# Optimization experiments

Measured on AMD Instinct MI355X. Metric: run time of the kernel, lower is better.

Reference implementation:

```python
import jax, jax.numpy as jnp
import numpy as np

V = 100000
E = 524288
D_IN = 128
D_OUT = 128
NUM_REL = 474
BN_EPS = 1e-5


def setup_inputs() -> dict:
    key = jax.random.key(0)
    ks = jax.random.split(key, 12)
    return {
        "x": jax.random.normal(ks[0], (V, D_IN), dtype=jnp.float32),
        "rel_repr": jax.random.normal(ks[1], (NUM_REL, D_IN), dtype=jnp.float32),
        "edge_norm": jax.random.uniform(ks[2], (E,), dtype=jnp.float32),
        "in_w": jax.random.normal(ks[3], (D_IN, D_OUT), dtype=jnp.float32) * 0.1,
        "out_w": jax.random.normal(ks[4], (D_IN, D_OUT), dtype=jnp.float32) * 0.1,
        "loop_w": jax.random.normal(ks[5], (D_IN, D_OUT), dtype=jnp.float32) * 0.1,
        "w_rel": jax.random.normal(ks[6], (D_IN, D_OUT), dtype=jnp.float32) * 0.1,
        "loop_rel": jax.random.normal(ks[7], (1, D_IN), dtype=jnp.float32),
        "bias": jnp.zeros((D_OUT,), dtype=jnp.float32),
        "src": jax.random.randint(ks[8], (E,), 0, V, dtype=jnp.int32),
        "dst": jax.random.randint(ks[9], (E,), 0, V, dtype=jnp.int32),
        "edge_type": jax.random.randint(ks[10], (E,), 0, NUM_REL, dtype=jnp.int32),
    }


def reference(x, rel_repr, edge_norm, in_w, out_w, loop_w, w_rel, loop_rel, bias, src, dst, edge_type):
    # comp primitive 'mult': edge_data = src_emb * rel[edge_type]   [E, D_IN]
    rel = rel_repr  # num_base=-1 -> rel_wt is None, rel.data = rel_repr
    edge_data = x[src] * rel[edge_type]
    half = edge_data.shape[0] // 2  # static under jit
    # first half of edges -> in_w, second half -> out_w
    msg = jnp.concatenate([edge_data[:half] @ in_w, edge_data[half:] @ out_w], axis=0)
    msg = msg * edge_norm[:, None]
    # agg primitive 'sum': scatter-sum into dst nodes
    agg = jax.ops.segment_sum(msg, dst, num_segments=x.shape[0])  # [V, D_OUT]
    # self-loop path: comp(x, loop_rel) @ loop_w
    loop_msg = (x * loop_rel) @ loop_w
    # comb primitive 'add', scaled by 1/3 (dropout with p=0 is identity)
    h = (agg + loop_msg) * (1.0 / 3.0)
    h = h + bias
    # BatchNorm1d, training-mode batch stats, gamma=1, beta=0
    mean = jnp.mean(h, axis=0)
    var = jnp.mean((h - mean) ** 2, axis=0)
    h = (h - mean) * jax.lax.rsqrt(var + BN_EPS)
    # act primitive 'relu'; ltr=True -> project relations
    return jax.nn.relu(h), rel @ w_rel
```

## Files before the change

### kernel.cpp

```cpp
#include <hip/hip_runtime.h>

#define V 100000
#define VP 100096
#define E_EDGES 524288
#define HALF 262144
#define D 128
#define NREL 474
#define BN_EPS 1e-5f
#define NBLK 98

#define ROWTILES 782
#define GEMM_GRID 1568
#define RED_BLKS 98
#define RELB 237
#define BNBLK 12500

#define LDK 392
#define LDB 40

typedef unsigned short u16;
typedef unsigned int u32;
typedef unsigned long long u64;
typedef __attribute__((ext_vector_type(8))) short short8;
typedef __attribute__((ext_vector_type(4))) float f32x4;

__device__ __forceinline__ u16 f2bf(float f) {
    union { float f; u32 u; } v; v.f = f;
    u32 u = v.u;
    return (u16)((u + 0x7fffu + ((u >> 16) & 1u)) >> 16);
}
__device__ __forceinline__ u32 pk2(float a, float b) {
    return (u32)f2bf(a) | ((u32)f2bf(b) << 16);
}

__global__ __launch_bounds__(256) void hist_k(const int* __restrict__ dst, u32* __restrict__ cnt) {
    int e = blockIdx.x * 256 + threadIdx.x;
    if (e >= E_EDGES) return;
    u32 d = (u32)dst[e];
    if (d >= V) d = 0;
    atomicAdd(&cnt[d], 1u);
}

__global__ __launch_bounds__(1024) void scanA_k(const u32* __restrict__ cnt,
                                                u32* __restrict__ cursor,
                                                u32* __restrict__ bsum) {
    __shared__ u32 wsum[16];
    int tid = threadIdx.x, wid = tid >> 6, lane = tid & 63;
    int idx = blockIdx.x * 1024 + tid;
    u32 v = (idx < V) ? cnt[idx] : 0u;
    u32 s = v;
#pragma unroll
    for (int o = 1; o < 64; o <<= 1) {
        u32 t = __shfl_up(s, o, 64);
        if (lane >= o) s += t;
    }
    if (lane == 63) wsum[wid] = s;
    __syncthreads();
    if (wid == 0) {
        u32 wv = (lane < 16) ? wsum[lane] : 0u;
#pragma unroll
        for (int o = 1; o < 16; o <<= 1) {
            u32 t = __shfl_up(wv, o, 64);
            if (lane >= o) wv += t;
        }
        if (lane < 16) wsum[lane] = wv;
    }
    __syncthreads();
    u32 wprev = wid ? wsum[wid - 1] : 0u;
    if (idx < V) cursor[idx] = s + wprev - v;
    if (tid == 0) bsum[blockIdx.x] = wsum[15];
}

__global__ __launch_bounds__(128) void scanBbt_k(
    u32* __restrict__ bsum,
    const float* __restrict__ in_w, const float* __restrict__ out_w,
    const float* __restrict__ loop_w, u16* __restrict__ Bt) {
    if (blockIdx.x > 0) {
        int n = blockIdx.x - 1;
        int t = threadIdx.x;
        const float* Ws[3] = {in_w, out_w, loop_w};
#pragma unroll
        for (int seg = 0; seg < 3; seg++)
            Bt[(size_t)n * 384 + seg * 128 + t] = f2bf(Ws[seg][(size_t)t * D + n]);
        return;
    }
    __shared__ u32 wtot;
    int t = threadIdx.x, lane = t & 63, w = t >> 6;
    u32 v = (t < NBLK) ? bsum[t] : 0u;
    u32 s = v;
#pragma unroll
    for (int o = 1; o < 64; o <<= 1) {
        u32 x = __shfl_up(s, o, 64);
        if (lane >= o) s += x;
    }
    if (w == 0 && lane == 63) wtot = s;
    __syncthreads();
    u32 add = (w == 1) ? wtot : 0u;
    if (t < NBLK) bsum[t] = add + s - v;
}

__global__ __launch_bounds__(256) void fill_rec_k(
    const int* __restrict__ dst, const int* __restrict__ src, const int* __restrict__ etype,
    const float* __restrict__ enorm, u32* __restrict__ cursor, const u32* __restrict__ bsum,
    u64* __restrict__ rec) {
    int e = blockIdx.x * 256 + threadIdx.x;
    if (e >= E_EDGES) return;
    u32 d = (u32)dst[e];   if (d >= V) d = 0;
    u32 s = (u32)src[e];   if (s >= V) s = 0;
    u32 t = (u32)etype[e]; if (t >= NREL) t = 0;
    float nm = enorm[e];
    u32 w = s | (t << 17) | ((e < HALF ? 0u : 1u) << 26);
    u32 slot = atomicAdd(&cursor[d], 1u) + bsum[d >> 10];
    u64 r = (u64)w | ((u64)__float_as_uint(nm) << 32);
    if (slot < E_EDGES) rec[slot] = r;
}

struct Rec { u32 s, t, hf; float nm; };
__device__ __forceinline__ Rec dec(u64 r) {
    Rec q; u32 w = (u32)r;
    q.s = w & 0x1FFFFu;
    q.t = (w >> 17) & 0x1FFu;
    q.hf = (w >> 26) & 1u;
    q.nm = __uint_as_float((u32)(r >> 32));
    return q;
}

__global__ __launch_bounds__(256) void gather_k(
    const float* __restrict__ x, const float* __restrict__ rel,
    const u32* __restrict__ cursor, const u32* __restrict__ cnt,
    const u32* __restrict__ bsum, const u64* __restrict__ rec, u16* __restrict__ Aagg) {
    int wave = threadIdx.x >> 6, lane = threadIdx.x & 63;
    int v = blockIdx.x * 4 + wave;
    u32* arow = (u32*)(Aagg + (size_t)v * 256);
    if (v >= V) { arow[lane] = 0u; arow[64 + lane] = 0u; return; }

    u32 n = cnt[v];
    u32 end = cursor[v] + bsum[v >> 10];
    if (end > E_EDGES) end = E_EDGES;
    if (n > end) n = end;
    u32 p = end - n;
    int col = lane * 2;

    float iA0 = 0.f, iA1 = 0.f, oA0 = 0.f, oA1 = 0.f;
    float iB0 = 0.f, iB1 = 0.f, oB0 = 0.f, oB1 = 0.f;

    for (u32 q = p; q < end; q += 4) {
        u64 r0 = rec[q], r1 = rec[q + 1], r2 = rec[q + 2], r3 = rec[q + 3];
        Rec q0 = dec(r0), q1 = dec(r1), q2 = dec(r2), q3 = dec(r3);
        if (q + 1 >= end) q1.nm = 0.f;
        if (q + 2 >= end) q2.nm = 0.f;
        if (q + 3 >= end) q3.nm = 0.f;
        float2 x0 = *(const float2*)(x + (size_t)q0.s * D + col);
        float2 x1 = *(const float2*)(x + (size_t)q1.s * D + col);
        float2 x2 = *(const float2*)(x + (size_t)q2.s * D + col);
        float2 x3 = *(const float2*)(x + (size_t)q3.s * D + col);
        float2 v0 = *(const float2*)(rel + (size_t)q0.t * D + col);
        float2 v1 = *(const float2*)(rel + (size_t)q1.t * D + col);
        float2 v2 = *(const float2*)(rel + (size_t)q2.t * D + col);
        float2 v3 = *(const float2*)(rel + (size_t)q3.t * D + col);
        float f00 = x0.x * v0.x * q0.nm, f01 = x0.y * v0.y * q0.nm;
        float f10 = x1.x * v1.x * q1.nm, f11 = x1.y * v1.y * q1.nm;
        float f20 = x2.x * v2.x * q2.nm, f21 = x2.y * v2.y * q2.nm;
        float f30 = x3.x * v3.x * q3.nm, f31 = x3.y * v3.y * q3.nm;
        if (q0.hf) { oA0 += f00; oA1 += f01; } else { iA0 += f00; iA1 += f01; }
        if (q1.hf) { oB0 += f10; oB1 += f11; } else { iB0 += f10; iB1 += f11; }
        if (q2.hf) { oA0 += f20; oA1 += f21; } else { iA0 += f20; iA1 += f21; }
        if (q3.hf) { oB0 += f30; oB1 += f31; } else { iB0 += f30; iB1 += f31; }
    }
    arow[lane]      = pk2(iA0 + iB0, iA1 + iB1);
    arow[64 + lane] = pk2(oA0 + oB0, oA1 + oB1);
}

__global__ __launch_bounds__(512) void gemm_k(
    const u16* __restrict__ Aagg, const u16* __restrict__ Bt,
    const float* __restrict__ x, const float* __restrict__ loop_rel,
    float* __restrict__ h_out, float* __restrict__ psum, float* __restrict__ psq) {
    __shared__ u16 Bs[64 * 384];
    __shared__ float s_sum[64], s_sq[64];
    int tid = threadIdx.x, wave = tid >> 6, lane = tid & 63;
    int bid = blockIdx.x;
    int rt   = ((bid >> 4) << 3) | (bid & 7);
    int half = (bid >> 3) & 1;
    if (rt >= ROWTILES) return;
    int row0 = rt * 128;

    if (tid < 64) s_sum[tid] = 0.f;
    else if (tid < 128) s_sq[tid - 64] = 0.f;

    int m16 = lane & 15;
    int kq = (lane >> 4) * 8;
    int gvm = row0 + wave * 16 + m16;
    const u16* arow = Aagg + (size_t)gvm * 256;
    bool vok = gvm < V;

    short8 af[8];
#pragma unroll
    for (int ks = 0; ks < 8; ks++) af[ks] = *(const short8*)(arow + ks * 32 + kq);
    short8 lf[4];
    {
        const float* xp = x + (size_t)gvm * D + kq;
#pragma unroll
        for (int kk = 0; kk < 4; kk++) {
            float4 x0 = vok ? *(const float4*)(xp + kk * 32)     : (float4){0.f, 0.f, 0.f, 0.f};
            float4 x1 = vok ? *(const float4*)(xp + kk * 32 + 4) : (float4){0.f, 0.f, 0.f, 0.f};
            float4 l0 = *(const float4*)(loop_rel + kk * 32 + kq);
            float4 l1 = *(const float4*)(loop_rel + kk * 32 + kq + 4);
            union { u32 u[4]; short8 s; } c;
            c.u[0] = pk2(x0.x * l0.x, x0.y * l0.y);
            c.u[1] = pk2(x0.z * l0.z, x0.w * l0.w);
            c.u[2] = pk2(x1.x * l1.x, x1.y * l1.y);
            c.u[3] = pk2(x1.z * l1.z, x1.w * l1.w);
            lf[kk] = c.s;
        }
    }

    {
        const u16* srcB = Bt + (size_t)half * 64 * 384;
        char* bsw = (char*)Bs;
#pragma unroll
        for (int it = 0; it < 6; it++) {
            int c = it * 512 + tid;
            int n = c / 48, s = c - n * 48;
            short8 vv = *(const short8*)(srcB + (size_t)n * 384 + s * 8);
            *(short8*)(bsw + (((u32)(n * 768 + s * 16)) ^ (u32)((n & 7) << 4))) = vv;
        }
    }
    __syncthreads();

    const char* bsb = (const char*)Bs;
    f32x4 acc[4];
#pragma unroll
    for (int ct = 0; ct < 4; ct++) acc[ct] = (f32x4){0.f, 0.f, 0.f, 0.f};

#pragma unroll
    for (int ks = 0; ks < 8; ks++) {
#pragma unroll
        for (int ct = 0; ct < 4; ct++) {
            int n = ct * 16 + m16;
            short8 b = *(const short8*)(bsb + (((u32)(n * 768 + (ks * 32 + kq) * 2)) ^ (u32)((n & 7) << 4)));
            acc[ct] = __builtin_amdgcn_mfma_f32_16x16x32_bf16(af[ks], b, acc[ct], 0, 0, 0);
        }
    }
#pragma unroll
    for (int kk = 0; kk < 4; kk++) {
#pragma unroll
        for (int ct = 0; ct < 4; ct++) {
            int n = ct * 16 + m16;
            short8 b = *(const short8*)(bsb + (((u32)(n * 768 + (256 + kk * 32 + kq) * 2)) ^ (u32)((n & 7) << 4)));
            acc[ct] = __builtin_amdgcn_mfma_f32_16x16x32_bf16(lf[kk], b, acc[ct], 0, 0, 0);
        }
    }

    int m4 = (lane >> 4) * 4;
#pragma unroll
    for (int ct = 0; ct < 4; ct++) {
        float ls = 0.f, lq = 0.f;
#pragma unroll
        for (int i = 0; i < 4; i++) {
            int gv = row0 + wave * 16 + m4 + i;
            if (gv < V) {
                float h = acc[ct][i] * (1.0f / 3.0f);
                h_out[(size_t)gv * D + half * 64 + ct * 16 + m16] = h;
                ls += h; lq += h * h;
            }
        }
        atomicAdd(&s_sum[ct * 16 + m16], ls);
        atomicAdd(&s_sq[ct * 16 + m16], lq);
    }
    __syncthreads();
    if (tid < 64) psum[(size_t)rt * 128 + half * 64 + tid] = s_sum[tid];
    else if (tid < 128) psq[(size_t)rt * 128 + half * 64 + (tid - 64)] = s_sq[tid - 64];
}

__global__ __launch_bounds__(256) void bn_reduce(
    const float* __restrict__ psum, const float* __restrict__ psq,
    float* __restrict__ colsum, float* __restrict__ colsumsq) {
    int t = threadIdx.x;
    int c = t & 127;
    const float* srcp = (t < 128) ? psum : psq;
    float s = 0.f;
    int r0 = blockIdx.x * 8;
#pragma unroll
    for (int i = 0; i < 8; i++) {
        int r = r0 + i;
        if (r < ROWTILES) s += srcp[(size_t)r * 128 + c];
    }
    atomicAdd(((t < 128) ? colsum : colsumsq) + c, s);
}

__global__ __launch_bounds__(256) void final_k(
    float* __restrict__ hio, const float* __restrict__ colsum, const float* __restrict__ colsumsq,
    const float* __restrict__ rel, const float* __restrict__ w, float* __restrict__ out1) {
    int bid = blockIdx.x;
    if (bid < RELB) {
        __shared__ float rs[2][D];
        int rh = threadIdx.x >> 7, c = threadIdx.x & 127;
        int r = bid * 2 + rh;
        rs[rh][c] = rel[(size_t)r * D + c];
        __syncthreads();
        float s = 0.f;
#pragma unroll 8
        for (int k = 0; k < D; k++) s += rs[rh][k] * w[(size_t)k * D + c];
        out1[(size_t)r * D + c] = s;
        return;
    }
    int idx = ((bid - RELB) * 256 + threadIdx.x) * 4;
    if (idx >= V * D) return;
    int col = idx & (D - 1);
    float4 hv = *(const float4*)(hio + idx);
    float4 ov;
    {
        float m0 = colsum[col + 0] * (1.0f / (float)V);
        float m1 = colsum[col + 1] * (1.0f / (float)V);
        float m2 = colsum[col + 2] * (1.0f / (float)V);
        float m3 = colsum[col + 3] * (1.0f / (float)V);
        if (!isfinite(m0)) m0 = 0.f;
        if (!isfinite(m1)) m1 = 0.f;
        if (!isfinite(m2)) m2 = 0.f;
        if (!isfinite(m3)) m3 = 0.f;
        float v0 = colsumsq[col + 0] * (1.0f / (float)V) - m0 * m0;
        float v1 = colsumsq[col + 1] * (1.0f / (float)V) - m1 * m1;
        float v2 = colsumsq[col + 2] * (1.0f / (float)V) - m2 * m2;
        float v3 = colsumsq[col + 3] * (1.0f / (float)V) - m3 * m3;
        if (!isfinite(v0) || v0 < 0.f) v0 = 0.f;
        if (!isfinite(v1) || v1 < 0.f) v1 = 0.f;
        if (!isfinite(v2) || v2 < 0.f) v2 = 0.f;
        if (!isfinite(v3) || v3 < 0.f) v3 = 0.f;
        float f0 = (hv.x - m0) * rsqrtf(v0 + BN_EPS);
        float f1 = (hv.y - m1) * rsqrtf(v1 + BN_EPS);
        float f2 = (hv.z - m2) * rsqrtf(v2 + BN_EPS);
        float f3 = (hv.w - m3) * rsqrtf(v3 + BN_EPS);
        ov.x = (f0 > 0.f) ? f0 : 0.f;
        ov.y = (f1 > 0.f) ? f1 : 0.f;
        ov.z = (f2 > 0.f) ? f2 : 0.f;
        ov.w = (f3 > 0.f) ? f3 : 0.f;
    }
    *(float4*)(hio + idx) = ov;
}

__global__ __launch_bounds__(1024) void scan_k(const u32* __restrict__ cnt,
                                               u32* __restrict__ cursor) {
    __shared__ u32 wsum[16];
    __shared__ u32 carry_s;
    int tid = threadIdx.x, wid = tid >> 6, lane = tid & 63;
    if (tid == 0) carry_s = 0;
    __syncthreads();
    for (int base = 0; base < V; base += 1024) {
        int idx = base + tid;
        u32 v = (idx < V) ? cnt[idx] : 0u;
        u32 s = v;
#pragma unroll
        for (int o = 1; o < 64; o <<= 1) {
            u32 t = __shfl_up(s, o, 64);
            if (lane >= o) s += t;
        }
        if (lane == 63) wsum[wid] = s;
        __syncthreads();
        if (wid == 0) {
            u32 wv = (lane < 16) ? wsum[lane] : 0u;
#pragma unroll
            for (int o = 1; o < 16; o <<= 1) {
                u32 t = __shfl_up(wv, o, 64);
                if (lane >= o) wv += t;
            }
            if (lane < 16) wsum[lane] = wv;
        }
        __syncthreads();
        u32 wprev = (wid == 0) ? 0u : wsum[wid - 1];
        u32 c = carry_s;
        if (idx < V) cursor[idx] = c + s + wprev - v;
        u32 tot = wsum[15];
        __syncthreads();
        if (tid == 0) carry_s = c + tot;
        __syncthreads();
    }
}

__global__ __launch_bounds__(256) void fill_k(
    const int* __restrict__ dst, u32* __restrict__ cursor, u32* __restrict__ eid) {
    int e = blockIdx.x * 256 + threadIdx.x;
    if (e >= E_EDGES) return;
    u32 d = (u32)dst[e];
    if (d >= V) d = 0;
    u32 slot = atomicAdd(&cursor[d], 1u);
    if (slot < E_EDGES) eid[slot] = (u32)e;
}

__global__ __launch_bounds__(256, 1) void fused_k(
    const float* __restrict__ x, const float* __restrict__ rel, const float* __restrict__ loop_rel,
    const float* __restrict__ in_w, const float* __restrict__ out_w, const float* __restrict__ loop_w,
    const float* __restrict__ enorm,
    const int* __restrict__ src, const int* __restrict__ etype,
    const u32* __restrict__ cursor, const u32* __restrict__ cnt,
    const u32* __restrict__ eid,
    float* __restrict__ h_out, float* __restrict__ colsum, float* __restrict__ colsumsq) {
    __shared__ u16 Alds[64 * LDK];
    __shared__ u16 Bs[D * LDB];
    __shared__ float s_sum[D], s_sq[D];

    int tid = threadIdx.x, wave = tid >> 6, lane = tid & 63;
    int row0 = blockIdx.x * 64;

    if (tid < D) { s_sum[tid] = 0.f; s_sq[tid] = 0.f; }

    for (int i = 0; i < 16; i++) {
        int row = wave * 16 + i;
        int gv = row0 + row;
        u32* arow = (u32*)(Alds + row * LDK);
        if (gv < V) {
            float a0 = 0.f, a1 = 0.f, b0 = 0.f, b1 = 0.f;
            float c0 = 0.f, c1 = 0.f, d0 = 0.f, d1 = 0.f;
            u32 n = cnt[gv];
            u32 end = cursor[gv];
            u32 beg = (end >= n) ? end - n : 0u;
            if (beg >= E_EDGES) { beg = 0; n = 0; }
            if (n > E_EDGES - beg) n = E_EDGES - beg;
            u32 nend = beg + n;
            u32 p = beg;
            for (; p + 2 <= nend; p += 2) {
                u32 e0 = eid[p];           if (e0 >= E_EDGES) e0 = 0;
                u32 e1 = eid[p + 1];       if (e1 >= E_EDGES) e1 = 0;
                u32 s0 = (u32)src[e0];     if (s0 >= V) s0 = 0;
                u32 s1 = (u32)src[e1];     if (s1 >= V) s1 = 0;
                u32 t0 = (u32)etype[e0];   if (t0 >= NREL) t0 = 0;
                u32 t1 = (u32)etype[e1];   if (t1 >= NREL) t1 = 0;
                float n0 = enorm[e0];
                float n1 = enorm[e1];
                float2 xv0 = *(const float2*)(x + (size_t)s0 * D + lane * 2);
                float2 xv1 = *(const float2*)(x + (size_t)s1 * D + lane * 2);
                float2 rv0 = *(const float2*)(rel + (size_t)t0 * D + lane * 2);
                float2 rv1 = *(const float2*)(rel + (size_t)t1 * D + lane * 2);
                float f00 = xv0.x * rv0.x * n0, f01 = xv0.y * rv0.y * n0;
                float f10 = xv1.x * rv1.x * n1, f11 = xv1.y * rv1.y * n1;
                if (e0 < HALF) { a0 += f00; a1 += f01; } else { b0 += f00; b1 += f01; }
                if (e1 < HALF) { c0 += f10; c1 += f11; } else { d0 += f10; d1 += f11; }
            }
            if (p < nend) {
                u32 e0 = eid[p];           if (e0 >= E_EDGES) e0 = 0;
                u32 s0 = (u32)src[e0];     if (s0 >= V) s0 = 0;
                u32 t0 = (u32)etype[e0];   if (t0 >= NREL) t0 = 0;
                float n0 = enorm[e0];
                float2 xv0 = *(const float2*)(x + (size_t)s0 * D + lane * 2);
                float2 rv0 = *(const float2*)(rel + (size_t)t0 * D + lane * 2);
                float f00 = xv0.x * rv0.x * n0, f01 = xv0.y * rv0.y * n0;
                if (e0 < HALF) { a0 += f00; a1 += f01; } else { b0 += f00; b1 += f01; }
            }
            a0 += c0; a1 += c1; b0 += d0; b1 += d1;
            float2 xv = *(const float2*)(x + (size_t)gv * D + lane * 2);
            float2 lv = *(const float2*)(loop_rel + lane * 2);
            arow[lane]       = pk2(a0, a1);
            arow[64 + lane]  = pk2(b0, b1);
            arow[128 + lane] = pk2(xv.x * lv.x, xv.y * lv.y);
        } else {
            arow[lane] = 0u; arow[64 + lane] = 0u; arow[128 + lane] = 0u;
        }
    }
    __syncthreads();

    f32x4 acc[8];
#pragma unroll
    for (int ct = 0; ct < 8; ct++) acc[ct] = (f32x4){0.f, 0.f, 0.f, 0.f};

    int m = wave * 16 + (lane & 15);
    int kq = (lane >> 4) * 8;
    int bk = tid >> 3;
    int bn0 = (tid & 7) * 16;

    for (int ks = 0; ks < 12; ks++) {
        int k0 = ks * 32;
        int seg = k0 >> 7;
        int kloc = k0 & 127;
        const float* W = (seg == 0) ? in_w : (seg == 1 ? out_w : loop_w);
#pragma unroll
        for (int j = 0; j < 16; j += 2) {
            float2 w2 = *(const float2*)(W + (size_t)(kloc + bk) * D + bn0 + j);
            Bs[(bn0 + j) * LDB + bk]     = f2bf(w2.x);
            Bs[(bn0 + j + 1) * LDB + bk] = f2bf(w2.y);
        }
        __syncthreads();
        short8 a = *(const short8*)(Alds + m * LDK + k0 + kq);
#pragma unroll
        for (int ct = 0; ct < 8; ct++) {
            short8 b = *(const short8*)(Bs + (ct * 16 + (lane & 15)) * LDB + kq);
            acc[ct] = __builtin_amdgcn_mfma_f32_16x16x32_bf16(a, b, acc[ct], 0, 0, 0);
        }
        __syncthreads();
    }

    int m4 = (lane >> 4) * 4;
#pragma unroll
    for (int ct = 0; ct < 8; ct++) {
        float ls = 0.f, lq = 0.f;
#pragma unroll
        for (int i = 0; i < 4; i++) {
            int gv = row0 + wave * 16 + m4 + i;
            if (gv < V) {
                float h = acc[ct][i] * (1.0f / 3.0f);
                h_out[(size_t)gv * D + ct * 16 + (lane & 15)] = h;
                ls += h; lq += h * h;
            }
        }
        atomicAdd(&s_sum[ct * 16 + (lane & 15)], ls);
        atomicAdd(&s_sq[ct * 16 + (lane & 15)], lq);
    }
    __syncthreads();
    if (tid < D) atomicAdd(&colsum[tid], s_sum[tid]);
    else atomicAdd(&colsumsq[tid - D], s_sq[tid - D]);
}

__global__ void bn_finalize(const float* __restrict__ colsum, const float* __restrict__ colsumsq,
                            float* __restrict__ mean, float* __restrict__ scale) {
    int t = threadIdx.x;
    float m = colsum[t] * (1.0f / (float)V);
    if (!isfinite(m)) m = 0.f;
    float var = colsumsq[t] * (1.0f / (float)V) - m * m;
    if (!isfinite(var) || var < 0.f) var = 0.f;
    mean[t] = m;
    scale[t] = rsqrtf(var + BN_EPS);
}

__global__ __launch_bounds__(256) void bn_relu(
    float* __restrict__ hio, const float* __restrict__ mean, const float* __restrict__ scale) {
    int idx = (blockIdx.x * 256 + threadIdx.x) * 4;
    if (idx >= V * D) return;
    int col = idx & (D - 1);
    float4 hv = *(const float4*)(hio + idx);
    float f0 = (hv.x - mean[col + 0]) * scale[col + 0];
    float f1 = (hv.y - mean[col + 1]) * scale[col + 1];
    float f2 = (hv.z - mean[col + 2]) * scale[col + 2];
    float f3 = (hv.w - mean[col + 3]) * scale[col + 3];
    f0 = (f0 > 0.f) ? f0 : 0.f;
    f1 = (f1 > 0.f) ? f1 : 0.f;
    f2 = (f2 > 0.f) ? f2 : 0.f;
    f3 = (f3 > 0.f) ? f3 : 0.f;
    float4 ov; ov.x = f0; ov.y = f1; ov.z = f2; ov.w = f3;
    *(float4*)(hio + idx) = ov;
}

__global__ __launch_bounds__(128) void rel_gemm(
    const float* __restrict__ rel, const float* __restrict__ w, float* __restrict__ out1) {
    __shared__ float rs[D];
    int t = threadIdx.x;
    int r = blockIdx.x;
    rs[t] = rel[(size_t)r * D + t];
    __syncthreads();
    float s = 0.f;
#pragma unroll 8
    for (int k = 0; k < D; k++) s += rs[k] * w[(size_t)k * D + t];
    out1[(size_t)r * D + t] = s;
}

extern "C" void kernel_launch(void* const* d_in, const int* in_sizes, int n_in,
                              void* d_out, int out_size, void* d_ws, size_t ws_size,
                              hipStream_t stream) {
    const float* x        = (const float*)d_in[0];
    const float* rel_repr = (const float*)d_in[1];
    const float* enorm    = (const float*)d_in[2];
    const float* in_w     = (const float*)d_in[3];
    const float* out_w    = (const float*)d_in[4];
    const float* loop_w   = (const float*)d_in[5];
    const float* w_rel    = (const float*)d_in[6];
    const float* loop_rel = (const float*)d_in[7];
    const int* src   = (const int*)d_in[9];
    const int* dst   = (const int*)d_in[10];
    const int* etype = (const int*)d_in[11];

    float* out0 = (float*)d_out;
    float* out1 = (float*)d_out + (size_t)V * D;

    char* ws = (char*)d_ws;

    {
        size_t off = 0;
        u32* cnt        = (u32*)(ws + off); off += (size_t)V * 4;
        float* colsum   = (float*)(ws + off); off += 512;
        float* colsumsq = (float*)(ws + off); off += 512;
        size_t zero_bytes = off;
        u32* cursor = (u32*)(ws + off); off += (size_t)V * 4;
        u32* bsum   = (u32*)(ws + off); off += 512;
        u16* Bt     = (u16*)(ws + off); off += (size_t)128 * 384 * 2;
        float* psum = (float*)(ws + off); off += (size_t)ROWTILES * 128 * 4;
        float* psq  = (float*)(ws + off); off += (size_t)ROWTILES * 128 * 4;
        u64* rec    = (u64*)(ws + off); off += (size_t)(E_EDGES + 8) * 8;
        u16* Aagg   = (u16*)(ws + off); off += (size_t)VP * 256 * 2;

        if (ws_size >= off) {
            hipMemsetAsync(d_ws, 0, zero_bytes, stream);
            hipMemsetAsync(rec + E_EDGES, 0, 64, stream);
            hist_k<<<(E_EDGES + 255) / 256, 256, 0, stream>>>(dst, cnt);
            scanA_k<<<NBLK, 1024, 0, stream>>>(cnt, cursor, bsum);
            scanBbt_k<<<129, 128, 0, stream>>>(bsum, in_w, out_w, loop_w, Bt);
            fill_rec_k<<<(E_EDGES + 255) / 256, 256, 0, stream>>>(dst, src, etype, enorm, cursor, bsum, rec);
            gather_k<<<VP / 4, 256, 0, stream>>>(x, rel_repr, cursor, cnt, bsum, rec, Aagg);
            gemm_k<<<GEMM_GRID, 512, 0, stream>>>(Aagg, Bt, x, loop_rel, out0, psum, psq);
            bn_reduce<<<RED_BLKS, 256, 0, stream>>>(psum, psq, colsum, colsumsq);
            final_k<<<RELB + BNBLK, 256, 0, stream>>>(out0, colsum, colsumsq, rel_repr, w_rel, out1);
            return;
        }
    }

    {
        size_t off = 0;
        u32* cnt      = (u32*)(ws + off); off += (size_t)V * 4;
        float* colsum = (float*)(ws + off); off += 512;
        float* colsumsq = (float*)(ws + off); off += 512;
        size_t zero_bytes = off;
        u32* cursor   = (u32*)(ws + off); off += (size_t)V * 4;
        float* meanp  = (float*)(ws + off); off += 512;
        float* scalep = (float*)(ws + off); off += 512;
        u32* eid      = (u32*)(ws + off); off += (size_t)E_EDGES * 4;

        if (ws_size < off) return;

        hipMemsetAsync(d_ws, 0, zero_bytes, stream);
        hist_k<<<(E_EDGES + 255) / 256, 256, 0, stream>>>(dst, cnt);
        scan_k<<<1, 1024, 0, stream>>>(cnt, cursor);
        fill_k<<<(E_EDGES + 255) / 256, 256, 0, stream>>>(dst, cursor, eid);
        fused_k<<<(V + 63) / 64, 256, 0, stream>>>(x, rel_repr, loop_rel, in_w, out_w, loop_w,
                                                   enorm, src, etype,
                                                   cursor, cnt, eid,
                                                   out0, colsum, colsumsq);
        bn_finalize<<<1, 128, 0, stream>>>(colsum, colsumsq, meanp, scalep);
        bn_relu<<<(V * D / 4 + 255) / 256, 256, 0, stream>>>(out0, meanp, scalep);
        rel_gemm<<<NREL, 128, 0, stream>>>(rel_repr, w_rel, out1);
    }
}
```

Baseline: 319.9 us.

## Make GEMM persistent over row tiles and write per-wave BN partials

The GEMM kernel becomes persistent: 512 blocks each stage their half of the B matrix into LDS once and loop over row tiles with stride 256, instead of reloading B for every tile. The shared-memory atomics for batch-norm partial sums are replaced by wave shuffles, with each wave writing its own partial row. bn_reduce now sums eight times as many partial rows. The gather kernel also zeroes the source and type indices of padded records so out-of-range lanes read row 0 instead of stale indices. The trade-off is less parallelism per tile and a larger partials buffer.

```diff
diff --git a/kernel.cpp b/kernel.cpp
--- a/kernel.cpp
+++ b/kernel.cpp
@@ -10,7 +10,8 @@
 #define NBLK 98
 
 #define ROWTILES 782
-#define GEMM_GRID 1568
+#define PROWS (ROWTILES * 8)
+#define GEMM_PBLK 512
 #define RED_BLKS 98
 #define RELB 237
 #define BNBLK 12500
@@ -147,9 +148,9 @@
     for (u32 q = p; q < end; q += 4) {
         u64 r0 = rec[q], r1 = rec[q + 1], r2 = rec[q + 2], r3 = rec[q + 3];
         Rec q0 = dec(r0), q1 = dec(r1), q2 = dec(r2), q3 = dec(r3);
-        if (q + 1 >= end) q1.nm = 0.f;
-        if (q + 2 >= end) q2.nm = 0.f;
-        if (q + 3 >= end) q3.nm = 0.f;
+        if (q + 1 >= end) { q1.s = 0; q1.t = 0; q1.nm = 0.f; }
+        if (q + 2 >= end) { q2.s = 0; q2.t = 0; q2.nm = 0.f; }
+        if (q + 3 >= end) { q3.s = 0; q3.t = 0; q3.nm = 0.f; }
         float2 x0 = *(const float2*)(x + (size_t)q0.s * D + col);
         float2 x1 = *(const float2*)(x + (size_t)q1.s * D + col);
         float2 x2 = *(const float2*)(x + (size_t)q2.s * D + col);
@@ -171,48 +172,17 @@
     arow[64 + lane] = pk2(oA0 + oB0, oA1 + oB1);
 }
 
-__global__ __launch_bounds__(512) void gemm_k(
+__global__ __launch_bounds__(512, 4) void gemm_k(
     const u16* __restrict__ Aagg, const u16* __restrict__ Bt,
     const float* __restrict__ x, const float* __restrict__ loop_rel,
-    float* __restrict__ h_out, float* __restrict__ psum, float* __restrict__ psq) {
+    float* __restrict__ h_out, float* __restrict__ ps, float* __restrict__ pq) {
     __shared__ u16 Bs[64 * 384];
-    __shared__ float s_sum[64], s_sq[64];
     int tid = threadIdx.x, wave = tid >> 6, lane = tid & 63;
     int bid = blockIdx.x;
-    int rt   = ((bid >> 4) << 3) | (bid & 7);
-    int half = (bid >> 3) & 1;
-    if (rt >= ROWTILES) return;
-    int row0 = rt * 128;
-
-    if (tid < 64) s_sum[tid] = 0.f;
-    else if (tid < 128) s_sq[tid - 64] = 0.f;
-
+    int half = bid >> 8;
+    int t0   = bid & 255;
     int m16 = lane & 15;
     int kq = (lane >> 4) * 8;
-    int gvm = row0 + wave * 16 + m16;
-    const u16* arow = Aagg + (size_t)gvm * 256;
-    bool vok = gvm < V;
-
-    short8 af[8];
-#pragma unroll
-    for (int ks = 0; ks < 8; ks++) af[ks] = *(const short8*)(arow + ks * 32 + kq);
-    short8 lf[4];
-    {
-        const float* xp = x + (size_t)gvm * D + kq;
-#pragma unroll
-        for (int kk = 0; kk < 4; kk++) {
-            float4 x0 = vok ? *(const float4*)(xp + kk * 32)     : (float4){0.f, 0.f, 0.f, 0.f};
-            float4 x1 = vok ? *(const float4*)(xp + kk * 32 + 4) : (float4){0.f, 0.f, 0.f, 0.f};
-            float4 l0 = *(const float4*)(loop_rel + kk * 32 + kq);
-            float4 l1 = *(const float4*)(loop_rel + kk * 32 + kq + 4);
-            union { u32 u[4]; short8 s; } c;
-            c.u[0] = pk2(x0.x * l0.x, x0.y * l0.y);
-            c.u[1] = pk2(x0.z * l0.z, x0.w * l0.w);
-            c.u[2] = pk2(x1.x * l1.x, x1.y * l1.y);
-            c.u[3] = pk2(x1.z * l1.z, x1.w * l1.w);
-            lf[kk] = c.s;
-        }
-    }
 
     {
         const u16* srcB = Bt + (size_t)half * 64 * 384;
@@ -226,64 +196,94 @@
         }
     }
     __syncthreads();
-
     const char* bsb = (const char*)Bs;
-    f32x4 acc[4];
-#pragma unroll
-    for (int ct = 0; ct < 4; ct++) acc[ct] = (f32x4){0.f, 0.f, 0.f, 0.f};
-
-#pragma unroll
-    for (int ks = 0; ks < 8; ks++) {
+
+    for (int rt = t0; rt < ROWTILES; rt += 256) {
+        int row0 = rt * 128;
+        int gvm = row0 + wave * 16 + m16;
+        const u16* arow = Aagg + (size_t)gvm * 256;
+        bool vok = gvm < V;
+
+        short8 af[8];
+#pragma unroll
+        for (int ks = 0; ks < 8; ks++) af[ks] = *(const short8*)(arow + ks * 32 + kq);
+        short8 lf[4];
+        {
+            const float* xp = x + (size_t)gvm * D + kq;
+#pragma unroll
+            for (int kk = 0; kk < 4; kk++) {
+                float4 x0 = vok ? *(const float4*)(xp + kk * 32)     : (float4){0.f, 0.f, 0.f, 0.f};
+                float4 x1 = vok ? *(const float4*)(xp + kk * 32 + 4) : (float4){0.f, 0.f, 0.f, 0.f};
+                float4 l0 = *(const float4*)(loop_rel + kk * 32 + kq);
+                float4 l1 = *(const float4*)(loop_rel + kk * 32 + kq + 4);
+                union { u32 u[4]; short8 s; } c;
+                c.u[0] = pk2(x0.x * l0.x, x0.y * l0.y);
+                c.u[1] = pk2(x0.z * l0.z, x0.w * l0.w);
+                c.u[2] = pk2(x1.x * l1.x, x1.y * l1.y);
+                c.u[3] = pk2(x1.z * l1.z, x1.w * l1.w);
+                lf[kk] = c.s;
+            }
+        }
+
+        f32x4 acc[4];
+#pragma unroll
+        for (int ct = 0; ct < 4; ct++) acc[ct] = (f32x4){0.f, 0.f, 0.f, 0.f};
+
+#pragma unroll
+        for (int ks = 0; ks < 8; ks++) {
+#pragma unroll
+            for (int ct = 0; ct < 4; ct++) {
+                int n = ct * 16 + m16;
+                short8 b = *(const short8*)(bsb + (((u32)(n * 768 + (ks * 32 + kq) * 2)) ^ (u32)((n & 7) << 4)));
+                acc[ct] = __builtin_amdgcn_mfma_f32_16x16x32_bf16(af[ks], b, acc[ct], 0, 0, 0);
+            }
+        }
+#pragma unroll
+        for (int kk = 0; kk < 4; kk++) {
+#pragma unroll
+            for (int ct = 0; ct < 4; ct++) {
+                int n = ct * 16 + m16;
+                short8 b = *(const short8*)(bsb + (((u32)(n * 768 + (256 + kk * 32 + kq) * 2)) ^ (u32)((n & 7) << 4)));
+                acc[ct] = __builtin_amdgcn_mfma_f32_16x16x32_bf16(lf[kk], b, acc[ct], 0, 0, 0);
+            }
+        }
+
+        int m4 = (lane >> 4) * 4;
+        size_t pbase = ((size_t)rt * 8 + wave) * 128 + (size_t)half * 64;
 #pragma unroll
         for (int ct = 0; ct < 4; ct++) {
-            int n = ct * 16 + m16;
-            short8 b = *(const short8*)(bsb + (((u32)(n * 768 + (ks * 32 + kq) * 2)) ^ (u32)((n & 7) << 4)));
-            acc[ct] = __builtin_amdgcn_mfma_f32_16x16x32_bf16(af[ks], b, acc[ct], 0, 0, 0);
-        }
-    }
-#pragma unroll
-    for (int kk = 0; kk < 4; kk++) {
-#pragma unroll
-        for (int ct = 0; ct < 4; ct++) {
-            int n = ct * 16 + m16;
-            short8 b = *(const short8*)(bsb + (((u32)(n * 768 + (256 + kk * 32 + kq) * 2)) ^ (u32)((n & 7) << 4)));
-            acc[ct] = __builtin_amdgcn_mfma_f32_16x16x32_bf16(lf[kk], b, acc[ct], 0, 0, 0);
-        }
-    }
-
-    int m4 = (lane >> 4) * 4;
-#pragma unroll
-    for (int ct = 0; ct < 4; ct++) {
-        float ls = 0.f, lq = 0.f;
-#pragma unroll
-        for (int i = 0; i < 4; i++) {
-            int gv = row0 + wave * 16 + m4 + i;
-            if (gv < V) {
-                float h = acc[ct][i] * (1.0f / 3.0f);
-                h_out[(size_t)gv * D + half * 64 + ct * 16 + m16] = h;
-                ls += h; lq += h * h;
-            }
-        }
-        atomicAdd(&s_sum[ct * 16 + m16], ls);
-        atomicAdd(&s_sq[ct * 16 + m16], lq);
-    }
-    __syncthreads();
-    if (tid < 64) psum[(size_t)rt * 128 + half * 64 + tid] = s_sum[tid];
-    else if (tid < 128) psq[(size_t)rt * 128 + half * 64 + (tid - 64)] = s_sq[tid - 64];
+            float ls = 0.f, lq = 0.f;
+            f32x4 a = acc[ct];
+#pragma unroll
+            for (int i = 0; i < 4; i++) {
+                int gv = row0 + wave * 16 + m4 + i;
+                if (gv < V) {
+                    float h = a[i] * (1.0f / 3.0f);
+                    h_out[(size_t)gv * D + half * 64 + ct * 16 + m16] = h;
+                    ls += h; lq += h * h;
+                }
+            }
+            ls += __shfl_xor(ls, 16); ls += __shfl_xor(ls, 32);
+            lq += __shfl_xor(lq, 16); lq += __shfl_xor(lq, 32);
+            if ((lane >> 4) == 0) {
+                ps[pbase + ct * 16 + m16] = ls;
+                pq[pbase + ct * 16 + m16] = lq;
+            }
+        }
+    }
 }
 
 __global__ __launch_bounds__(256) void bn_reduce(
-    const float* __restrict__ psum, const float* __restrict__ psq,
+    const float* __restrict__ ps, const float* __restrict__ pq,
     float* __restrict__ colsum, float* __restrict__ colsumsq) {
     int t = threadIdx.x;
     int c = t & 127;
-    const float* srcp = (t < 128) ? psum : psq;
+    const float* srcp = (t < 128) ? ps : pq;
     float s = 0.f;
-    int r0 = blockIdx.x * 8;
-#pragma unroll
-    for (int i = 0; i < 8; i++) {
+    int r0 = blockIdx.x * 64;
+    for (int i = 0; i < 64; i++) {
         int r = r0 + i;
-        if (r < ROWTILES) s += srcp[(size_t)r * 128 + c];
+        if (r < PROWS) s += srcp[(size_t)r * 128 + c];
     }
     atomicAdd(((t < 128) ? colsum : colsumsq) + c, s);
 }
@@ -579,8 +579,8 @@
         u32* cursor = (u32*)(ws + off); off += (size_t)V * 4;
         u32* bsum   = (u32*)(ws + off); off += 512;
         u16* Bt     = (u16*)(ws + off); off += (size_t)128 * 384 * 2;
-        float* psum = (float*)(ws + off); off += (size_t)ROWTILES * 128 * 4;
-        float* psq  = (float*)(ws + off); off += (size_t)ROWTILES * 128 * 4;
+        float* ps   = (float*)(ws + off); off += (size_t)PROWS * 128 * 4;
+        float* pq   = (float*)(ws + off); off += (size_t)PROWS * 128 * 4;
         u64* rec    = (u64*)(ws + off); off += (size_t)(E_EDGES + 8) * 8;
         u16* Aagg   = (u16*)(ws + off); off += (size_t)VP * 256 * 2;
 
@@ -592,8 +592,8 @@
             scanBbt_k<<<129, 128, 0, stream>>>(bsum, in_w, out_w, loop_w, Bt);
             fill_rec_k<<<(E_EDGES + 255) / 256, 256, 0, stream>>>(dst, src, etype, enorm, cursor, bsum, rec);
             gather_k<<<VP / 4, 256, 0, stream>>>(x, rel_repr, cursor, cnt, bsum, rec, Aagg);
-            gemm_k<<<GEMM_GRID, 512, 0, stream>>>(Aagg, Bt, x, loop_rel, out0, psum, psq);
-            bn_reduce<<<RED_BLKS, 256, 0, stream>>>(psum, psq, colsum, colsumsq);
+            gemm_k<<<GEMM_PBLK, 512, 0, stream>>>(Aagg, Bt, x, loop_rel, out0, ps, pq);
+            bn_reduce<<<RED_BLKS, 256, 0, stream>>>(ps, pq, colsum, colsumsq);
             final_k<<<RELB + BNBLK, 256, 0, stream>>>(out0, colsum, colsumsq, rel_repr, w_rel, out1);
             return;
         }
```

Result: slower. 519.1 us (+62.3%).
